# Performance work log

Measured on AMD Instinct MI355X. Metric: run time of the kernel, lower is better.

## Reference

```python
import jax, jax.numpy as jnp
import numpy as np

BLOCK = 32  # GGML quantization block size (Q4_0 style)
Q_OFFSET = 8.0  # 4-bit values stored unsigned in [0,16), centered by -8


def setup_inputs() -> dict:
    key = jax.random.key(0)
    k1, k2, k3, k4, k5, k6 = jax.random.split(key, 6)
    O, I, R, T = 4096, 4096, 16, 8192
    x = jax.random.normal(k1, (T, I), dtype=jnp.float32)
    qweight = jax.random.randint(k2, (O, I), 0, 16, dtype=jnp.int32)
    scales = jax.random.uniform(k3, (O, I // BLOCK), dtype=jnp.float32)
    lora_a = jax.random.normal(k4, (O, R), dtype=jnp.float32)
    lora_b = jax.random.normal(k5, (R, I), dtype=jnp.float32)
    bias = jax.random.normal(k6, (O,), dtype=jnp.float32)
    return {"x": x, "qweight": qweight, "scales": scales,
            "lora_a": lora_a, "lora_b": lora_b, "bias": bias}


def reference(x, qweight, scales, lora_a, lora_b, bias):
    # --- dequantize_tensor: per-block scale * centered int codes ---
    O, I = qweight.shape
    q = qweight.astype(jnp.float32) - Q_OFFSET            # [O, I]
    w = (q.reshape(O, I // BLOCK, BLOCK) * scales[:, :, None]).reshape(O, I)
    # --- patch application (LoRA-style additive patch) ---
    w = w + lora_a @ lora_b                               # [O, I]
    # --- downstream consumption: linear layer ---
    y = x @ w.T + bias                                    # [T, O]
    return y
```

## Files before the change

### kernel.cpp

```cpp
#include <hip/hip_runtime.h>
#include <hip/hip_bf16.h>

typedef unsigned short u16;
typedef __attribute__((ext_vector_type(4))) float f32x4;
typedef __attribute__((ext_vector_type(8))) short bf16x8;
typedef __attribute__((ext_vector_type(8))) u16 u16x8;

#define GLDS16(g, l) __builtin_amdgcn_global_load_lds( \
    (const __attribute__((address_space(1))) void*)(g), \
    (__attribute__((address_space(3))) void*)(l), 16, 0, 0)

__device__ inline u16 f2bf(float f) {
  union { float f; unsigned u; } v; v.f = f;
  unsigned r = v.u + 0x7fffu + ((v.u >> 16) & 1u);
  return (u16)(r >> 16);
}

__global__ __launch_bounds__(256) void k_dequant_lora(
    const int* __restrict__ qw, const float* __restrict__ sc,
    const float* __restrict__ la, const float* __restrict__ lb,
    u16* __restrict__ W)
{
  const int I = 4096, R = 16;
  __shared__ float lbs[16][512];
  __shared__ float las[256];
  const int c0 = blockIdx.x * 512;
  const int o0 = blockIdx.y * 16;
  const int tid = threadIdx.x;

  las[tid] = la[(size_t)(o0 + (tid >> 4)) * R + (tid & 15)];
  #pragma unroll
  for (int i = 0; i < 8; ++i) {
    int idx = tid + i * 256;
    int r = idx >> 7;
    int cc4 = (idx & 127) << 2;
    *(float4*)&lbs[r][cc4] = *(const float4*)&lb[(size_t)r * I + c0 + cc4];
  }
  __syncthreads();

  const int cc = (tid & 63) * 8;
  const int rg = tid >> 6;
  #pragma unroll
  for (int rr = 0; rr < 4; ++rr) {
    const int o = o0 + rg * 4 + rr;
    float acc[8] = {0.f,0.f,0.f,0.f,0.f,0.f,0.f,0.f};
    #pragma unroll
    for (int r = 0; r < 16; ++r) {
      float av = las[(rg * 4 + rr) * 16 + r];
      float4 b0 = *(const float4*)&lbs[r][cc];
      float4 b1 = *(const float4*)&lbs[r][cc + 4];
      acc[0] += av * b0.x; acc[1] += av * b0.y;
      acc[2] += av * b0.z; acc[3] += av * b0.w;
      acc[4] += av * b1.x; acc[5] += av * b1.y;
      acc[6] += av * b1.z; acc[7] += av * b1.w;
    }
    const int4* qp = (const int4*)&qw[(size_t)o * I + c0 + cc];
    int4 q0 = qp[0], q1 = qp[1];
    float s = sc[(size_t)o * (I / 32) + ((c0 + cc) >> 5)];
    u16x8 w;
    w[0] = f2bf(((float)q0.x - 8.0f) * s + acc[0]);
    w[1] = f2bf(((float)q0.y - 8.0f) * s + acc[1]);
    w[2] = f2bf(((float)q0.z - 8.0f) * s + acc[2]);
    w[3] = f2bf(((float)q0.w - 8.0f) * s + acc[3]);
    w[4] = f2bf(((float)q1.x - 8.0f) * s + acc[4]);
    w[5] = f2bf(((float)q1.y - 8.0f) * s + acc[5]);
    w[6] = f2bf(((float)q1.z - 8.0f) * s + acc[6]);
    w[7] = f2bf(((float)q1.w - 8.0f) * s + acc[7]);
    *(u16x8*)&W[(size_t)o * I + c0 + cc] = w;
  }
}

__global__ __launch_bounds__(256) void k_cvt(const float* __restrict__ x,
                                             u16* __restrict__ xb)
{
  const size_t n = (size_t)8192 * 4096;
  const size_t stride = (size_t)gridDim.x * 256 * 8;
  for (size_t i = ((size_t)blockIdx.x * 256 + threadIdx.x) * 8; i < n; i += stride) {
    float4 a = *(const float4*)&x[i];
    float4 b = *(const float4*)&x[i + 4];
    u16x8 o;
    o[0] = f2bf(a.x); o[1] = f2bf(a.y); o[2] = f2bf(a.z); o[3] = f2bf(a.w);
    o[4] = f2bf(b.x); o[5] = f2bf(b.y); o[6] = f2bf(b.z); o[7] = f2bf(b.w);
    *(u16x8*)&xb[i] = o;
  }
}

__global__ __launch_bounds__(512, 2) void k_gemm(
    const u16* __restrict__ A, const u16* __restrict__ B,
    const float* __restrict__ bias, float* __restrict__ C)
{
  const int N = 4096, K = 4096;
  const int NTK = 128;
  __shared__ u16 As[4 * 8192];
  __shared__ u16 Bs[4 * 8192];

  const int bid = blockIdx.x;
  const int swz = (bid & 7) * 64 + (bid >> 3);
  const int m0 = (swz >> 4) * 256;
  const int n0 = (swz & 15) * 256;

  const int tid = threadIdx.x;
  const int wid = tid >> 6, lane = tid & 63;
  const int wid_m = wid >> 2, wid_n = wid & 3;

  const int st0 = wid;
  const int st1 = 8 + wid;
  const int srow = lane >> 2;
  const int schunk = (((lane & 3) ^ (((lane >> 5) & 1) << 1))) * 8;
  const u16* Asrc0 = A + (size_t)(m0 + st0 * 16 + srow) * K + schunk;
  const u16* Asrc1 = A + (size_t)(m0 + st1 * 16 + srow) * K + schunk;
  const u16* Bsrc0 = B + (size_t)(n0 + st0 * 16 + srow) * K + schunk;
  const u16* Bsrc1 = B + (size_t)(n0 + st1 * 16 + srow) * K + schunk;

#define STAGE_A(buf, t) do { \
    GLDS16(Asrc0 + (size_t)(t) * 32, &As[(buf) * 8192 + st0 * 512]); \
    GLDS16(Asrc1 + (size_t)(t) * 32, &As[(buf) * 8192 + st1 * 512]); } while (0)
#define STAGE_B(buf, t) do { \
    GLDS16(Bsrc0 + (size_t)(t) * 32, &Bs[(buf) * 8192 + st0 * 512]); \
    GLDS16(Bsrc1 + (size_t)(t) * 32, &Bs[(buf) * 8192 + st1 * 512]); } while (0)

  const int LA = (lane & 15) * 32 + (((lane >> 4) * 8) ^ ((lane & 8) ? 16 : 0));
  const int wmb = wid_m * 8;
  const int wnb = wid_n * 4;

  f32x4 acc[8][4] = {};
  bf16x8 aC[4], aN[4], bA[4], bB[4];

  STAGE_A(0, 0); STAGE_B(0, 0);
  STAGE_A(1, 1); STAGE_B(1, 1);
  asm volatile("s_waitcnt vmcnt(4)" ::: "memory");
  __builtin_amdgcn_s_barrier();
  __builtin_amdgcn_sched_barrier(0);
  #pragma unroll
  for (int m = 0; m < 4; ++m)
    aC[m] = *(const bf16x8*)&As[(wmb + m) * 512 + LA];
  #pragma unroll
  for (int n = 0; n < 4; ++n)
    bA[n] = *(const bf16x8*)&Bs[(wnb + n) * 512 + LA];

#define TILE(T, BCUR, BNXT) do { \
    const int b_ = (T) & 3; \
    const int bn_ = ((T) + 1) & 3; \
    _Pragma("unroll") \
    for (int m = 0; m < 4; ++m) \
      aN[m] = *(const bf16x8*)&As[b_ * 8192 + (wmb + 4 + m) * 512 + LA]; \
    if ((T) + 2 < NTK) STAGE_A(((T) + 2) & 3, (T) + 2); \
    __builtin_amdgcn_sched_barrier(0); \
    __builtin_amdgcn_s_setprio(1); \
    _Pragma("unroll") \
    for (int m = 0; m < 4; ++m) { \
      _Pragma("unroll") \
      for (int n = 0; n < 4; ++n) \
        acc[m][n] = __builtin_amdgcn_mfma_f32_16x16x32_bf16(aC[m], BCUR[n], acc[m][n], 0, 0, 0); \
    } \
    __builtin_amdgcn_s_setprio(0); \
    __builtin_amdgcn_sched_barrier(0); \
    if ((T) + 2 < NTK) { \
      STAGE_B(((T) + 2) & 3, (T) + 2); \
      asm volatile("s_waitcnt vmcnt(4)" ::: "memory"); \
    } else { \
      asm volatile("s_waitcnt vmcnt(0)" ::: "memory"); \
    } \
    __builtin_amdgcn_s_barrier(); \
    __builtin_amdgcn_sched_barrier(0); \
    if ((T) + 1 < NTK) { \
      _Pragma("unroll") \
      for (int m = 0; m < 4; ++m) \
        aC[m] = *(const bf16x8*)&As[bn_ * 8192 + (wmb + m) * 512 + LA]; \
      _Pragma("unroll") \
      for (int n = 0; n < 4; ++n) \
        BNXT[n] = *(const bf16x8*)&Bs[bn_ * 8192 + (wnb + n) * 512 + LA]; \
    } \
    __builtin_amdgcn_sched_barrier(0); \
    __builtin_amdgcn_s_setprio(1); \
    _Pragma("unroll") \
    for (int m = 0; m < 4; ++m) { \
      _Pragma("unroll") \
      for (int n = 0; n < 4; ++n) \
        acc[4 + m][n] = __builtin_amdgcn_mfma_f32_16x16x32_bf16(aN[m], BCUR[n], acc[4 + m][n], 0, 0, 0); \
    } \
    __builtin_amdgcn_s_setprio(0); \
    __builtin_amdgcn_sched_barrier(0); \
  } while (0)

  for (int t = 0; t < NTK; t += 2) {
    TILE(t, bA, bB);
    TILE(t + 1, bB, bA);
  }
#undef TILE
#undef STAGE_A
#undef STAGE_B

  const int crow = m0 + wid_m * 128 + ((lane >> 4) << 2);
  const int ccol = n0 + wid_n * 64 + (lane & 15);
  #pragma unroll
  for (int n = 0; n < 4; ++n) {
    float bv = bias[ccol + n * 16];
    #pragma unroll
    for (int m = 0; m < 8; ++m) {
      #pragma unroll
      for (int j = 0; j < 4; ++j) {
        C[(size_t)(crow + m * 16 + j) * N + ccol + n * 16] = acc[m][n][j] + bv;
      }
    }
  }
}

extern "C" void kernel_launch(void* const* d_in, const int* in_sizes, int n_in,
                              void* d_out, int out_size, void* d_ws, size_t ws_size,
                              hipStream_t stream) {
  const float* x    = (const float*)d_in[0];
  const int*   qw   = (const int*)d_in[1];
  const float* sc   = (const float*)d_in[2];
  const float* la   = (const float*)d_in[3];
  const float* lb   = (const float*)d_in[4];
  const float* bias = (const float*)d_in[5];
  float* y = (float*)d_out;

  u16* W  = (u16*)d_ws;
  u16* Xb = (u16*)((char*)d_ws + (size_t)32 * 1024 * 1024);

  dim3 gridD(4096 / 512, 4096 / 16);
  k_dequant_lora<<<gridD, 256, 0, stream>>>(qw, sc, la, lb, W);
  k_cvt<<<2048, 256, 0, stream>>>(x, Xb);
  const int ngemm = (8192 / 256) * (4096 / 256);
  k_gemm<<<ngemm, 512, 0, stream>>>(Xb, W, bias, y);
}
```

Baseline: 357.4 us.

## Switch GEMM to 32x32x16 bf16 MFMA tiles with remapped LDS fragments

Replaces the 16x16x32 MFMA instructions with 32x32x16 bf16 MFMAs, so each wave holds 4x2 accumulator tiles of 16 floats instead of 8x4 tiles of 4. The LDS fragment addressing and the output epilogue are remapped to the 32x32 layout. Launch bounds drop to one block per SIMD and some sched_barriers are removed or moved. The larger MFMA shape is meant to cut instruction-issue overhead and LDS reads per FLOP. In exchange, occupancy hints drop and the fragment mapping must be exactly right for correctness.

```diff
diff --git a/kernel.cpp b/kernel.cpp
--- a/kernel.cpp
+++ b/kernel.cpp
@@ -2,7 +2,7 @@
 #include <hip/hip_bf16.h>
 
 typedef unsigned short u16;
-typedef __attribute__((ext_vector_type(4))) float f32x4;
+typedef __attribute__((ext_vector_type(16))) float f32x16;
 typedef __attribute__((ext_vector_type(8))) short bf16x8;
 typedef __attribute__((ext_vector_type(8))) u16 u16x8;
 
@@ -85,7 +85,7 @@
   }
 }
 
-__global__ __launch_bounds__(512, 2) void k_gemm(
+__global__ __launch_bounds__(512, 1) void k_gemm(
     const u16* __restrict__ A, const u16* __restrict__ B,
     const float* __restrict__ bias, float* __restrict__ C)
 {
@@ -119,11 +119,12 @@
     GLDS16(Bsrc0 + (size_t)(t) * 32, &Bs[(buf) * 8192 + st0 * 512]); \
     GLDS16(Bsrc1 + (size_t)(t) * 32, &Bs[(buf) * 8192 + st1 * 512]); } while (0)
 
-  const int LA = (lane & 15) * 32 + (((lane >> 4) * 8) ^ ((lane & 8) ? 16 : 0));
+  const int LA = ((lane >> 4) & 1) * 512 + (lane & 15) * 32 +
+                 (((lane >> 5) * 8) ^ ((lane & 8) ? 16 : 0));
   const int wmb = wid_m * 8;
   const int wnb = wid_n * 4;
 
-  f32x4 acc[8][4] = {};
+  f32x16 acc[4][2] = {};
   bf16x8 aC[4], aN[4], bA[4], bB[4];
 
   STAGE_A(0, 0); STAGE_B(0, 0);
@@ -132,55 +133,71 @@
   __builtin_amdgcn_s_barrier();
   __builtin_amdgcn_sched_barrier(0);
   #pragma unroll
-  for (int m = 0; m < 4; ++m)
-    aC[m] = *(const bf16x8*)&As[(wmb + m) * 512 + LA];
-  #pragma unroll
-  for (int n = 0; n < 4; ++n)
-    bA[n] = *(const bf16x8*)&Bs[(wnb + n) * 512 + LA];
+  for (int mi = 0; mi < 2; ++mi)
+    #pragma unroll
+    for (int ks = 0; ks < 2; ++ks)
+      aC[mi * 2 + ks] = *(const bf16x8*)&As[(wmb + mi * 2) * 512 + (LA ^ (ks << 4))];
+  #pragma unroll
+  for (int ni = 0; ni < 2; ++ni)
+    #pragma unroll
+    for (int ks = 0; ks < 2; ++ks)
+      bA[ni * 2 + ks] = *(const bf16x8*)&Bs[(wnb + ni * 2) * 512 + (LA ^ (ks << 4))];
 
 #define TILE(T, BCUR, BNXT) do { \
     const int b_ = (T) & 3; \
     const int bn_ = ((T) + 1) & 3; \
     _Pragma("unroll") \
-    for (int m = 0; m < 4; ++m) \
-      aN[m] = *(const bf16x8*)&As[b_ * 8192 + (wmb + 4 + m) * 512 + LA]; \
+    for (int mi = 0; mi < 2; ++mi) { \
+      _Pragma("unroll") \
+      for (int ks = 0; ks < 2; ++ks) \
+        aN[mi * 2 + ks] = *(const bf16x8*)&As[b_ * 8192 + (wmb + 4 + mi * 2) * 512 + (LA ^ (ks << 4))]; \
+    } \
     if ((T) + 2 < NTK) STAGE_A(((T) + 2) & 3, (T) + 2); \
-    __builtin_amdgcn_sched_barrier(0); \
     __builtin_amdgcn_s_setprio(1); \
     _Pragma("unroll") \
-    for (int m = 0; m < 4; ++m) { \
-      _Pragma("unroll") \
-      for (int n = 0; n < 4; ++n) \
-        acc[m][n] = __builtin_amdgcn_mfma_f32_16x16x32_bf16(aC[m], BCUR[n], acc[m][n], 0, 0, 0); \
+    for (int ks = 0; ks < 2; ++ks) { \
+      _Pragma("unroll") \
+      for (int mi = 0; mi < 2; ++mi) { \
+        _Pragma("unroll") \
+        for (int ni = 0; ni < 2; ++ni) \
+          acc[mi][ni] = __builtin_amdgcn_mfma_f32_32x32x16_bf16(aC[mi * 2 + ks], BCUR[ni * 2 + ks], acc[mi][ni], 0, 0, 0); \
+      } \
     } \
     __builtin_amdgcn_s_setprio(0); \
-    __builtin_amdgcn_sched_barrier(0); \
     if ((T) + 2 < NTK) { \
       STAGE_B(((T) + 2) & 3, (T) + 2); \
       asm volatile("s_waitcnt vmcnt(4)" ::: "memory"); \
     } else { \
       asm volatile("s_waitcnt vmcnt(0)" ::: "memory"); \
     } \
+    __builtin_amdgcn_sched_barrier(0); \
     __builtin_amdgcn_s_barrier(); \
     __builtin_amdgcn_sched_barrier(0); \
     if ((T) + 1 < NTK) { \
       _Pragma("unroll") \
-      for (int m = 0; m < 4; ++m) \
-        aC[m] = *(const bf16x8*)&As[bn_ * 8192 + (wmb + m) * 512 + LA]; \
-      _Pragma("unroll") \
-      for (int n = 0; n < 4; ++n) \
-        BNXT[n] = *(const bf16x8*)&Bs[bn_ * 8192 + (wnb + n) * 512 + LA]; \
-    } \
-    __builtin_amdgcn_sched_barrier(0); \
+      for (int mi = 0; mi < 2; ++mi) { \
+        _Pragma("unroll") \
+        for (int ks = 0; ks < 2; ++ks) \
+          aC[mi * 2 + ks] = *(const bf16x8*)&As[bn_ * 8192 + (wmb + mi * 2) * 512 + (LA ^ (ks << 4))]; \
+      } \
+      _Pragma("unroll") \
+      for (int ni = 0; ni < 2; ++ni) { \
+        _Pragma("unroll") \
+        for (int ks = 0; ks < 2; ++ks) \
+          BNXT[ni * 2 + ks] = *(const bf16x8*)&Bs[bn_ * 8192 + (wnb + ni * 2) * 512 + (LA ^ (ks << 4))]; \
+      } \
+    } \
     __builtin_amdgcn_s_setprio(1); \
     _Pragma("unroll") \
-    for (int m = 0; m < 4; ++m) { \
-      _Pragma("unroll") \
-      for (int n = 0; n < 4; ++n) \
-        acc[4 + m][n] = __builtin_amdgcn_mfma_f32_16x16x32_bf16(aN[m], BCUR[n], acc[4 + m][n], 0, 0, 0); \
+    for (int ks = 0; ks < 2; ++ks) { \
+      _Pragma("unroll") \
+      for (int mi = 0; mi < 2; ++mi) { \
+        _Pragma("unroll") \
+        for (int ni = 0; ni < 2; ++ni) \
+          acc[2 + mi][ni] = __builtin_amdgcn_mfma_f32_32x32x16_bf16(aN[mi * 2 + ks], BCUR[ni * 2 + ks], acc[2 + mi][ni], 0, 0, 0); \
+      } \
     } \
     __builtin_amdgcn_s_setprio(0); \
-    __builtin_amdgcn_sched_barrier(0); \
   } while (0)
 
   for (int t = 0; t < NTK; t += 2) {
@@ -191,16 +208,17 @@
 #undef STAGE_A
 #undef STAGE_B
 
-  const int crow = m0 + wid_m * 128 + ((lane >> 4) << 2);
-  const int ccol = n0 + wid_n * 64 + (lane & 15);
-  #pragma unroll
-  for (int n = 0; n < 4; ++n) {
-    float bv = bias[ccol + n * 16];
-    #pragma unroll
-    for (int m = 0; m < 8; ++m) {
+  const int crow0 = m0 + wid_m * 128 + ((lane >> 5) << 2);
+  const int ccol = n0 + wid_n * 64 + (lane & 31);
+  #pragma unroll
+  for (int ni = 0; ni < 2; ++ni) {
+    float bv = bias[ccol + ni * 32];
+    #pragma unroll
+    for (int mi = 0; mi < 4; ++mi) {
       #pragma unroll
-      for (int j = 0; j < 4; ++j) {
-        C[(size_t)(crow + m * 16 + j) * N + ccol + n * 16] = acc[m][n][j] + bv;
+      for (int reg = 0; reg < 16; ++reg) {
+        int row = crow0 + mi * 32 + (reg & 3) + ((reg >> 2) << 3);
+        C[(size_t)row * N + ccol + ni * 32] = acc[mi][ni][reg] + bv;
       }
     }
   }
```

Result: slower. 382.8 us (+7.1%).
